# Optimization experiments

Hardware: AMD Instinct MI355X
Metric: run time of the kernel (lower is better)

## Reference

```python
import jax, jax.numpy as jnp
import numpy as np

N, E, NG = 50000, 800000, 500          # nodes, edges, graphs
HID, HEADS, DH, AIN = 128, 4, 32, 200  # hidden, heads, head dim, atom feat dim
L, NBASE = 5, 1                        # total Roost layers; base layers = roost_layers-3 = 1


def _bn(x, g, b):
    # BatchNorm1d in training mode: batch stats over axis 0 (biased var), affine
    m = x.mean(axis=0)
    v = x.var(axis=0)
    return g * (x - m) * jax.lax.rsqrt(v + 1e-5) + b


def _mlp(x, W, b, g, be):
    # MLPLayer = Linear -> BatchNorm1d -> SiLU
    return jax.nn.silu(_bn(x @ W + b, g, be))


def _roost(x, w, src, dst, Wf, bf, gf, bef, Wg, bg, gg, beg, gn, ben):
    n = x.shape[0]
    hihj = jnp.concatenate([x[src], x[dst]], axis=-1)            # [E, 2h]
    e = jnp.exp(_mlp(hihj, Wf, bf, gf, bef))                     # [E, 1]
    wexp = w[src] * e                                            # [E, 1] src weight * exp(e_ij)
    sum_w = jax.ops.segment_sum(wexp, dst, num_segments=n)       # [N, 1] dst-normalizer
    a = wexp / sum_w[dst]                                        # [E, 1] attention coeff
    z = jnp.einsum('ef,hfd->ehd', hihj, Wg) + bg                 # [E, H, dh] per-head linear
    z = jax.nn.silu(gg * (z - z.mean(axis=0)) * jax.lax.rsqrt(z.var(axis=0) + 1e-5) + beg)
    m = (a[:, :, None] * z).reshape(hihj.shape[0], HID)          # concat heads -> [E, h]
    h = jax.ops.segment_sum(m, dst, num_segments=n)              # scatter-sum to dst nodes
    return _bn(h, gn, ben) + x                                   # bn_nodes + residual


def setup_inputs() -> dict:
    ks = list(jax.random.split(jax.random.key(0), 16))
    f32 = jnp.float32
    return {
        "atom_features": jax.random.normal(ks[0], (N, AIN), f32),
        "node_weight": jax.random.uniform(ks[1], (N, 1), f32, minval=0.05, maxval=1.0),
        "eps": jax.random.normal(ks[2], (N, HID), f32),
        "src": jax.random.randint(ks[3], (E,), 0, N),
        "dst": jax.random.randint(ks[4], (E,), 0, N),
        "graph_ids": jnp.sort(jax.random.randint(ks[5], (N,), 0, NG)),
        "W_embed": jax.random.normal(ks[6], (AIN, HID), f32) / np.sqrt(AIN).astype(np.float32),
        "b_embed": jnp.zeros((HID,), f32),
        "g_embed": jnp.ones((HID,), f32),
        "be_embed": jnp.zeros((HID,), f32),
        "Wf": jax.random.normal(ks[7], (L, 2 * HID, 1), f32) / np.sqrt(2 * HID).astype(np.float32),
        "bf": jnp.zeros((L, 1), f32),
        "gf": jnp.ones((L, 1), f32),
        "bef": jnp.zeros((L, 1), f32),
        "Wg": jax.random.normal(ks[8], (L, HEADS, 2 * HID, DH), f32) / np.sqrt(2 * HID).astype(np.float32),
        "bg": jnp.zeros((L, HEADS, DH), f32),
        "gg": jnp.ones((L, HEADS, DH), f32),
        "beg": jnp.zeros((L, HEADS, DH), f32),
        "gn": jnp.ones((L, HID), f32),
        "ben": jnp.zeros((L, HID), f32),
        "W_mu": jax.random.normal(ks[9], (HID, HID), f32) / np.sqrt(HID).astype(np.float32),
        "b_mu": jnp.zeros((HID,), f32),
        "W_var": jax.random.normal(ks[10], (HID, HID), f32) * 0.01,
        "b_var": jnp.zeros((HID,), f32),
    }


def reference(atom_features, node_weight, eps, W_embed, b_embed, g_embed, be_embed,
              Wf, bf, gf, bef, Wg, bg, gg, beg, gn, ben,
              W_mu, b_mu, W_var, b_var, src, dst, graph_ids):
    x = _mlp(atom_features, W_embed, b_embed, g_embed, be_embed)  # atom_embedding
    for i in range(NBASE):                                        # base_modules
        x = _roost(x, node_weight, src, dst, Wf[i], bf[i], gf[i], bef[i],
                   Wg[i], bg[i], gg[i], beg[i], gn[i], ben[i])
    mu = x @ W_mu + b_mu
    logvar = x @ W_var + b_var
    x = eps * jnp.exp(0.5 * logvar) + mu                          # reparameterize
    for i in range(NBASE, L):                                     # module_layers
        x = _roost(x, node_weight, src, dst, Wf[i], bf[i], gf[i], bef[i],
                   Wg[i], bg[i], gg[i], beg[i], gn[i], ben[i])
    sums = jax.ops.segment_sum(x, graph_ids, num_segments=NG)     # AvgPooling
    cnt = jax.ops.segment_sum(jnp.ones((N,), x.dtype), graph_ids, num_segments=NG)
    xr = sums / jnp.maximum(cnt, 1.0)[:, None]
    kld = jnp.mean(-0.5 * jnp.sum(1.0 + logvar - mu * mu - jnp.exp(logvar), axis=1))
    return xr, kld
```

## Files before the change

kernel.cpp:

```cpp
#include <hip/hip_runtime.h>
#include <hip/hip_bf16.h>
#include <stdint.h>

#define HID 128
#define LAYERS 5

typedef __attribute__((ext_vector_type(8))) short short8;
typedef __attribute__((ext_vector_type(4))) float f32x4;

__device__ __forceinline__ float bf2f(unsigned int u16) {
  union { unsigned int i; float f; } c; c.i = u16 << 16; return c.f;
}
__device__ __forceinline__ unsigned short f2bf(float f) {
  union { float f; unsigned int i; } c; c.f = f;
  unsigned int r = c.i + 0x7fffu + ((c.i >> 16) & 1u);
  return (unsigned short)(r >> 16);
}
__device__ __forceinline__ float fexp(float x) {
  float r; asm("v_exp_f32 %0, %1" : "=v"(r) : "v"(x * 1.44269504f)); return r;
}
__device__ __forceinline__ float frcp(float x) {
  float r; asm("v_rcp_f32 %0, %1" : "=v"(r) : "v"(x)); return r;
}
__device__ __forceinline__ float siluf(float v) { return v * frcp(1.f + fexp(-v)); }

template<int KS, int NCT, bool BF16OUT>
__launch_bounds__(256)
__global__ void gemm_bf16_kernel(const unsigned short* __restrict__ A,
                                 const unsigned short* __restrict__ Bt,
                                 const float* __restrict__ bias,
                                 void* __restrict__ Cv, int M) {
  constexpr int K = KS * 32;
  constexpr int SLOTS = KS * 4;
  constexpr int SSTR = (SLOTS + 7) & ~7;
  __shared__ unsigned short wlds[NCT * 16 * SSTR * 8];
  for (int i = threadIdx.x; i < NCT * 16 * SLOTS; i += 256) {
    int col = i / SLOTS, slot = i % SLOTS;
    int phys = slot ^ (col & 7);
    *(uint4*)&wlds[(col * SSTR + phys) * 8] = *(const uint4*)(Bt + (size_t)col * K + slot * 8);
  }
  __syncthreads();
  int lane = threadIdx.x & 63, wid = threadIdx.x >> 6;
  int l15 = lane & 15, l4 = lane >> 4;
  int n0 = blockIdx.x * 64 + wid * 16;
  f32x4 acc[NCT];
  #pragma unroll
  for (int ct = 0; ct < NCT; ++ct) { f32x4 z = {0.f, 0.f, 0.f, 0.f}; acc[ct] = z; }
  int ar = n0 + l15; if (ar >= M) ar = M - 1;
  #pragma unroll
  for (int kk = 0; kk < KS; ++kk) {
    short8 af = *(const short8*)(A + (size_t)ar * K + kk * 32 + l4 * 8);
    #pragma unroll
    for (int ct = 0; ct < NCT; ++ct) {
      int col = ct * 16 + l15;
      int phys = (kk * 4 + l4) ^ (col & 7);
      short8 bfr = *(const short8*)&wlds[(col * SSTR + phys) * 8];
      acc[ct] = __builtin_amdgcn_mfma_f32_16x16x32_bf16(af, bfr, acc[ct], 0, 0, 0);
    }
  }
  #pragma unroll
  for (int ct = 0; ct < NCT; ++ct) {
    int col = ct * 16 + l15;
    #pragma unroll
    for (int j = 0; j < 4; ++j) {
      int n = n0 + l4 * 4 + j;
      if (n < M) {
        float v = acc[ct][j] + bias[col];
        if (BF16OUT) ((unsigned short*)Cv)[(size_t)n * (NCT * 16) + col] = f2bf(v);
        else         ((float*)Cv)[(size_t)n * (NCT * 16) + col] = v;
      }
    }
  }
}

__global__ void cast_atom_kernel(const float* __restrict__ atom, unsigned short* __restrict__ ab,
                                 int N, int AIN) {
  int n = blockIdx.x, k = threadIdx.x;
  if (n < N && k < 224)
    ab[(size_t)n * 224 + k] = f2bf(k < AIN ? atom[(size_t)n * AIN + k] : 0.f);
}
__global__ void prep_we_kernel(const float* __restrict__ W, unsigned short* __restrict__ Bt,
                               int AIN) {
  int i = blockIdx.x * 256 + threadIdx.x;
  if (i >= 128 * 224) return;
  int col = i / 224, k = i % 224;
  Bt[i] = f2bf(k < AIN ? W[(size_t)k * 128 + col] : 0.f);
}

__global__ void colstats_kernel(const float* __restrict__ in, int M, float* __restrict__ stats) {
  int f = threadIdx.x & 127;
  int rl = threadIdx.x >> 7;
  float s = 0, s2 = 0;
  for (int r = blockIdx.x * 2 + rl; r < M; r += gridDim.x * 2) {
    float v = in[(size_t)r * 128 + f];
    s += v; s2 += v * v;
  }
  __shared__ float l1[256], l2[256];
  l1[threadIdx.x] = s; l2[threadIdx.x] = s2;
  __syncthreads();
  if (rl == 0) {
    atomicAdd(&stats[f],       s  + l1[128 + f]);
    atomicAdd(&stats[128 + f], s2 + l2[128 + f]);
  }
}

template<bool SILU, bool RES>
__global__ void bn_act_kernel(const float* __restrict__ in, const float* __restrict__ stats,
                              const float* __restrict__ g, const float* __restrict__ be,
                              const float* __restrict__ resid, float invM,
                              float* __restrict__ xout, unsigned short* __restrict__ xbout,
                              size_t total) {
  int f = threadIdx.x & 127;
  float mean = stats[f] * invM;
  float var  = stats[128 + f] * invM - mean * mean;
  float sc = g[f] * rsqrtf(var + 1e-5f);
  float sh = be[f] - mean * sc;
  for (size_t i = (size_t)blockIdx.x * blockDim.x + threadIdx.x; i < total;
       i += (size_t)gridDim.x * blockDim.x) {
    float v = in[i] * sc + sh;
    if (SILU) v = siluf(v);
    if (RES)  v += resid[i];
    xout[i] = v;
    xbout[i] = f2bf(v);
  }
}

__global__ void hist_kernel(const int* __restrict__ ids, int* __restrict__ deg, int E) {
  for (int e = blockIdx.x * blockDim.x + threadIdx.x; e < E; e += gridDim.x * blockDim.x)
    atomicAdd(&deg[ids[e]], 1);
}

__global__ void scan_block_kernel(const int* __restrict__ in, int n,
                                  int* __restrict__ excl, int* __restrict__ totals) {
  __shared__ int tmp[256];
  int idx = blockIdx.x * 256 + threadIdx.x;
  int v = (idx < n) ? in[idx] : 0;
  tmp[threadIdx.x] = v;
  __syncthreads();
  for (int o = 1; o < 256; o <<= 1) {
    int t = (threadIdx.x >= o) ? tmp[threadIdx.x - o] : 0;
    __syncthreads();
    tmp[threadIdx.x] += t;
    __syncthreads();
  }
  if (idx < n) excl[idx] = tmp[threadIdx.x] - v;
  if (threadIdx.x == 255 && totals) totals[blockIdx.x] = tmp[255];
}

__global__ void scan_add_kernel(const int* __restrict__ excl, const int* __restrict__ tot_excl,
                                const int* __restrict__ indeg, int* __restrict__ cstart, int n) {
  int idx = blockIdx.x * 256 + threadIdx.x;
  if (idx < n) {
    int v = excl[idx] + tot_excl[blockIdx.x];
    cstart[idx] = v;
    if (idx == n - 1) cstart[n] = v + indeg[idx];
  }
}

__global__ void scatter_kernel(const int* __restrict__ src, const int* __restrict__ dst,
                               const int* __restrict__ cstart, int* __restrict__ fill,
                               int* __restrict__ csrc, int* __restrict__ cdst, int E) {
  for (int e = blockIdx.x * blockDim.x + threadIdx.x; e < E; e += gridDim.x * blockDim.x) {
    int d = dst[e];
    int pos = cstart[d] + atomicAdd(&fill[d], 1);
    csrc[pos] = src[e];
    cdst[pos] = d;
  }
}

__global__ void prep_wg_kernel(const float* __restrict__ WgL, const float* __restrict__ bgL,
                               unsigned short* __restrict__ Bt, float* __restrict__ bias) {
  int i = blockIdx.x * 256 + threadIdx.x;
  if (i < 256 * 128) {
    int col = i >> 7, k = i & 127;
    int c = col & 127, h = c >> 5, d = c & 31;
    int krow = (col < 128) ? k : 128 + k;
    Bt[i] = f2bf(WgL[((size_t)h * 256 + krow) * 32 + d]);
  }
  if (i < 256) bias[i] = (i < 128) ? 0.f : bgL[i - 128];
}

__global__ void prep_mv_kernel(const float* __restrict__ Wm, const float* __restrict__ Wv,
                               const float* __restrict__ bm, const float* __restrict__ bv,
                               unsigned short* __restrict__ Bt, float* __restrict__ bias) {
  int i = blockIdx.x * 256 + threadIdx.x;
  if (i < 256 * 128) {
    int col = i >> 7, k = i & 127;
    Bt[i] = f2bf(col < 128 ? Wm[(size_t)k * 128 + col] : Wv[(size_t)k * 128 + col - 128]);
  }
  if (i < 256) bias[i] = (i < 128) ? bm[i] : bv[i - 128];
}

__global__ void pq_kernel(const unsigned short* __restrict__ xb, const float* __restrict__ WfL,
                          const float* __restrict__ bfL, const int* __restrict__ indeg,
                          const int* __restrict__ outdeg, float* __restrict__ p,
                          float* __restrict__ q, float* __restrict__ gstats, int N) {
  __shared__ float wf[256];
  __shared__ float red1[4], red2[4];
  wf[threadIdx.x] = WfL[threadIdx.x];
  __syncthreads();
  int wid = threadIdx.x >> 6, lane = threadIdx.x & 63;
  int f0 = lane * 2;
  float bf0 = bfL[0];
  float t1 = 0, t2 = 0;
  for (int n = blockIdx.x * 4 + wid; n < N; n += gridDim.x * 4) {
    unsigned xv = *(const unsigned*)(xb + ((size_t)n << 7) + f0);
    float x0 = bf2f(xv & 0xffffu), x1 = bf2f(xv >> 16);
    float pp = x0 * wf[f0]       + x1 * wf[f0 + 1];
    float qq = x0 * wf[128 + f0] + x1 * wf[129 + f0];
    #pragma unroll
    for (int o = 32; o; o >>= 1) { pp += __shfl_down(pp, o); qq += __shfl_down(qq, o); }
    if (lane == 0) {
      qq += bf0;
      p[n] = pp; q[n] = qq;
      float od = (float)outdeg[n], id = (float)indeg[n];
      t1 += od * pp + id * qq;
      t2 += od * pp * pp + id * qq * qq;
    }
  }
  if (lane == 0) { red1[wid] = t1; red2[wid] = t2; }
  __syncthreads();
  if (threadIdx.x == 0) {
    atomicAdd(&gstats[0], red1[0] + red1[1] + red1[2] + red1[3]);
    atomicAdd(&gstats[1], red2[0] + red2[1] + red2[2] + red2[3]);
  }
}

__global__ void zstat_node_kernel(const unsigned short* __restrict__ UVb,
                                  const int* __restrict__ indeg, const int* __restrict__ outdeg,
                                  float* __restrict__ zstats, int N) {
  int lane = threadIdx.x & 63, g = threadIdx.x >> 6;
  int f0 = lane * 2, f1 = f0 + 1;
  float zs0 = 0, zq0 = 0, zs1 = 0, zq1 = 0;
  for (int n = blockIdx.x * 4 + g; n < N; n += gridDim.x * 4) {
    float od = (float)outdeg[n], id = (float)indeg[n];
    unsigned up = *(const unsigned*)(UVb + ((size_t)n << 8) + f0);
    unsigned vp = *(const unsigned*)(UVb + ((size_t)n << 8) + 128 + f0);
    float u0 = bf2f(up & 0xffffu), u1 = bf2f(up >> 16);
    float v0 = bf2f(vp & 0xffffu), v1 = bf2f(vp >> 16);
    zs0 += od * u0 + id * v0;  zq0 += od * u0 * u0 + id * v0 * v0;
    zs1 += od * u1 + id * v1;  zq1 += od * u1 * u1 + id * v1 * v1;
  }
  __shared__ float r1[4][128], r2[4][128];
  r1[g][f0] = zs0; r1[g][f1] = zs1;
  r2[g][f0] = zq0; r2[g][f1] = zq1;
  __syncthreads();
  if (threadIdx.x < 128) {
    int f = threadIdx.x;
    atomicAdd(&zstats[f],       r1[0][f] + r1[1][f] + r1[2][f] + r1[3][f]);
    atomicAdd(&zstats[128 + f], r2[0][f] + r2[1][f] + r2[2][f] + r2[3][f]);
  }
}

__global__ void xwalk_kernel(const unsigned short* __restrict__ UVb,
                             const int* __restrict__ csrc, const int* __restrict__ cdst,
                             const float* __restrict__ p, const float* __restrict__ q,
                             float* __restrict__ zc_parts, float* __restrict__ gc_parts, int E) {
  int lane = threadIdx.x & 63, wid = threadIdx.x >> 6;
  int gw = (blockIdx.x * 256 + threadIdx.x) >> 6;
  int nw = (gridDim.x * 256) >> 6;
  int f0 = lane * 2;
  float cr0 = 0, cr1 = 0, gc = 0;
  int nch = (E + 63) >> 6;
  for (int c = gw; c < nch; c += nw) {
    int e0 = c << 6, len = min(64, E - e0);
    int ee = e0 + (lane < len ? lane : len - 1);
    int idxs = csrc[ee], idxd = cdst[ee];
    if (lane < len) gc += p[idxs] * q[idxd];
    int dcur = __shfl(idxd, 0);
    float su0 = 0, su1 = 0;
    const unsigned short* base = UVb;
    #define LDU(i) (*(const unsigned*)(base + ((size_t)__shfl(idxs, (i) < len ? (i) : len - 1) << 8) + f0))
    unsigned a0 = LDU(0), a1 = LDU(1), a2 = LDU(2), a3 = LDU(3);
    for (int bs = 0; bs < len; bs += 4) {
      unsigned b0 = LDU(bs + 4), b1 = LDU(bs + 5), b2 = LDU(bs + 6), b3 = LDU(bs + 7);
      #define PROCX(i, up) if ((i) < len) {                                        \
        int d = __shfl(idxd, (i));                                                 \
        if (d != dcur) {                                                           \
          unsigned vp = *(const unsigned*)(base + ((size_t)dcur << 8) + 128 + f0); \
          cr0 += bf2f(vp & 0xffffu) * su0; cr1 += bf2f(vp >> 16) * su1;            \
          su0 = su1 = 0; dcur = d;                                                 \
        }                                                                          \
        su0 += bf2f((up) & 0xffffu); su1 += bf2f((up) >> 16); }
      PROCX(bs + 0, a0); PROCX(bs + 1, a1); PROCX(bs + 2, a2); PROCX(bs + 3, a3);
      a0 = b0; a1 = b1; a2 = b2; a3 = b3;
    }
    unsigned vp = *(const unsigned*)(base + ((size_t)dcur << 8) + 128 + f0);
    cr0 += bf2f(vp & 0xffffu) * su0; cr1 += bf2f(vp >> 16) * su1;
    #undef PROCX
    #undef LDU
  }
  __shared__ float r1[4][128], rg[4];
  #pragma unroll
  for (int o = 32; o; o >>= 1) gc += __shfl_down(gc, o);
  if (lane == 0) rg[wid] = gc;
  r1[wid][f0] = cr0; r1[wid][f0 + 1] = cr1;
  __syncthreads();
  if (threadIdx.x < 128) {
    int f = threadIdx.x;
    atomicAdd(&zc_parts[(blockIdx.x & 31) * 128 + f], r1[0][f] + r1[1][f] + r1[2][f] + r1[3][f]);
  }
  if (threadIdx.x == 0)
    atomicAdd(&gc_parts[blockIdx.x & 31], rg[0] + rg[1] + rg[2] + rg[3]);
}

__global__ void gate_wexp_kernel(const int* __restrict__ csrc, const int* __restrict__ cdst,
                                 const float* __restrict__ p, const float* __restrict__ q,
                                 const float* __restrict__ nodew, const float* __restrict__ gstats,
                                 const float* __restrict__ gc_parts,
                                 const float* __restrict__ gfL, const float* __restrict__ befL,
                                 float* __restrict__ wexp, float* __restrict__ sum_w,
                                 int E, float invE) {
  float gcr = 0;
  #pragma unroll
  for (int i = 0; i < 32; ++i) gcr += gc_parts[i];
  float gm  = gstats[0] * invE;
  float gv  = (gstats[1] + 2.f * gcr) * invE - gm * gm;
  float gsc = gfL[0] * rsqrtf(gv + 1e-5f);
  float gsh = befL[0] - gm * gsc;
  for (int e = blockIdx.x * blockDim.x + threadIdx.x; e < E; e += gridDim.x * blockDim.x) {
    int s = csrc[e], d = cdst[e];
    float v = (p[s] + q[d]) * gsc + gsh;
    v = v * frcp(1.f + fexp(-v));
    float we = nodew[s] * fexp(v);
    wexp[e] = we;
    atomicAdd(&sum_w[d], we);
  }
}

__global__ void walk2_kernel(const unsigned short* __restrict__ UVb,
                             const int* __restrict__ csrc, const int* __restrict__ cdst,
                             const float* __restrict__ wexp, const float* __restrict__ sum_w,
                             const float* __restrict__ zstats, const float* __restrict__ zc_parts,
                             const float* __restrict__ gg, const float* __restrict__ beg,
                             float* __restrict__ h, int E, float invE) {
  int lane = threadIdx.x & 63;
  int gw = (blockIdx.x * 256 + threadIdx.x) >> 6;
  int nw = (gridDim.x * 256) >> 6;
  int f0 = lane * 2, f1 = f0 + 1;
  float cr0 = 0, cr1 = 0;
  #pragma unroll
  for (int i2 = 0; i2 < 32; ++i2) { cr0 += zc_parts[i2 * 128 + f0]; cr1 += zc_parts[i2 * 128 + f1]; }
  float zm0 = zstats[f0] * invE;
  float zv0 = (zstats[128 + f0] + 2.f * cr0) * invE - zm0 * zm0;
  float sc0 = gg[f0] * rsqrtf(zv0 + 1e-5f), sh0 = beg[f0] - zm0 * sc0;
  float zm1 = zstats[f1] * invE;
  float zv1 = (zstats[128 + f1] + 2.f * cr1) * invE - zm1 * zm1;
  float sc1 = gg[f1] * rsqrtf(zv1 + 1e-5f), sh1 = beg[f1] - zm1 * sc1;

  int nch = (E + 63) >> 6;
  for (int c = gw; c < nch; c += nw) {
    int e0 = c << 6, len = min(64, E - e0);
    int ee = e0 + (lane < len ? lane : len - 1);
    int idxs = csrc[ee], idxd = cdst[ee];
    float wv = wexp[ee];
    int dcur = __shfl(idxd, 0);
    float inv = frcp(sum_w[dcur]);
    float c0, c1;
    { unsigned vp = *(const unsigned*)(UVb + ((size_t)dcur << 8) + 128 + f0);
      c0 = bf2f(vp & 0xffffu) * sc0 + sh0; c1 = bf2f(vp >> 16) * sc1 + sh1; }
    float h0 = 0, h1 = 0;
    #define LDU(i) (*(const unsigned*)(UVb + ((size_t)__shfl(idxs, (i) < len ? (i) : len - 1) << 8) + f0))
    unsigned a0 = LDU(0), a1 = LDU(1), a2 = LDU(2), a3 = LDU(3);
    for (int bs = 0; bs < len; bs += 4) {
      unsigned b0 = LDU(bs + 4), b1 = LDU(bs + 5), b2 = LDU(bs + 6), b3 = LDU(bs + 7);
      #define PROCW(i, up) if ((i) < len) {                                          \
        int d = __shfl(idxd, (i));                                                   \
        float a = __shfl(wv, (i));                                                   \
        if (d != dcur) {                                                             \
          atomicAdd(&h[((size_t)dcur << 7) + f0], h0 * inv);                         \
          atomicAdd(&h[((size_t)dcur << 7) + f1], h1 * inv);                         \
          h0 = h1 = 0; dcur = d; inv = frcp(sum_w[d]);                               \
          unsigned vp = *(const unsigned*)(UVb + ((size_t)d << 8) + 128 + f0);       \
          c0 = bf2f(vp & 0xffffu) * sc0 + sh0; c1 = bf2f(vp >> 16) * sc1 + sh1;      \
        }                                                                            \
        float v0 = bf2f((up) & 0xffffu) * sc0 + c0;                                  \
        float v1 = bf2f((up) >> 16)     * sc1 + c1;                                  \
        v0 = v0 * frcp(1.f + fexp(-v0));                                             \
        v1 = v1 * frcp(1.f + fexp(-v1));                                             \
        h0 += a * v0; h1 += a * v1; }
      PROCW(bs + 0, a0); PROCW(bs + 1, a1); PROCW(bs + 2, a2); PROCW(bs + 3, a3);
      a0 = b0; a1 = b1; a2 = b2; a3 = b3;
    }
    atomicAdd(&h[((size_t)dcur << 7) + f0], h0 * inv);
    atomicAdd(&h[((size_t)dcur << 7) + f1], h1 * inv);
    #undef PROCW
    #undef LDU
  }
}

__global__ void reparam_kernel(const unsigned short* __restrict__ muv,
                               const float* __restrict__ eps,
                               float* __restrict__ x, unsigned short* __restrict__ xb,
                               float* __restrict__ kacc, size_t total) {
  float part = 0;
  for (size_t i = (size_t)blockIdx.x * blockDim.x + threadIdx.x; i < total;
       i += (size_t)gridDim.x * blockDim.x) {
    size_t n = i >> 7; int f = (int)(i & 127);
    float m = bf2f(muv[(n << 8) + f]);
    float l = bf2f(muv[(n << 8) + 128 + f]);
    float el = fexp(l);
    float v = eps[i] * fexp(0.5f * l) + m;
    x[i] = v;
    xb[i] = f2bf(v);
    part += 1.f + l - m * m - el;
  }
  #pragma unroll
  for (int o = 32; o; o >>= 1) part += __shfl_down(part, o);
  __shared__ float la[4];
  int lane = threadIdx.x & 63, wid = threadIdx.x >> 6;
  if (lane == 0) la[wid] = part;
  __syncthreads();
  if (threadIdx.x == 0) atomicAdd(kacc, la[0] + la[1] + la[2] + la[3]);
}

__global__ void pool_kernel(const float* __restrict__ x, const int* __restrict__ gid,
                            float* __restrict__ pools, float* __restrict__ cnt, int N) {
  int lane = threadIdx.x & 63;
  int gw = (blockIdx.x * 256 + threadIdx.x) >> 6;
  int nw = (gridDim.x * 256) >> 6;
  int f0 = lane * 2, f1 = f0 + 1;
  const int CH = 64;
  int nch = (N + CH - 1) / CH;
  for (int c = gw; c < nch; c += nw) {
    int n0 = c * CH, n1 = min(N, n0 + CH);
    int gcur = gid[n0];
    float a0 = 0, a1 = 0, count = 0;
    for (int n = n0; n < n1; ++n) {
      int g = gid[n];
      if (g != gcur) {
        atomicAdd(&pools[((size_t)gcur << 7) + f0], a0);
        atomicAdd(&pools[((size_t)gcur << 7) + f1], a1);
        if (lane == 0) atomicAdd(&cnt[gcur], count);
        a0 = a1 = 0; count = 0; gcur = g;
      }
      float2 xv = *(const float2*)(x + ((size_t)n << 7) + f0);
      a0 += xv.x; a1 += xv.y; count += 1.f;
    }
    atomicAdd(&pools[((size_t)gcur << 7) + f0], a0);
    atomicAdd(&pools[((size_t)gcur << 7) + f1], a1);
    if (lane == 0) atomicAdd(&cnt[gcur], count);
  }
}

__global__ void finalize_kernel(const float* __restrict__ pools, const float* __restrict__ cnt,
                                const float* __restrict__ kacc, float* __restrict__ out,
                                int NG, float invN) {
  int i = blockIdx.x * blockDim.x + threadIdx.x;
  if (i < NG * 128) {
    float c = cnt[i >> 7];
    c = c > 1.f ? c : 1.f;
    out[i] = pools[i] / c;
  }
  if (i == 0) out[NG * 128] = -0.5f * kacc[0] * invN;
}

extern "C" void kernel_launch(void* const* d_in, const int* in_sizes, int n_in,
                              void* d_out, int out_size, void* d_ws, size_t ws_size,
                              hipStream_t stream) {
  const float* atom    = (const float*)d_in[0];
  const float* nodew   = (const float*)d_in[1];
  const float* epsp    = (const float*)d_in[2];
  const int*   src     = (const int*)d_in[3];
  const int*   dst     = (const int*)d_in[4];
  const int*   gid     = (const int*)d_in[5];
  const float* W_embed = (const float*)d_in[6];
  const float* b_embed = (const float*)d_in[7];
  const float* g_embed = (const float*)d_in[8];
  const float* be_embed= (const float*)d_in[9];
  const float* Wf      = (const float*)d_in[10];
  const float* bfp     = (const float*)d_in[11];
  const float* gfp     = (const float*)d_in[12];
  const float* befp    = (const float*)d_in[13];
  const float* Wg      = (const float*)d_in[14];
  const float* bg      = (const float*)d_in[15];
  const float* gg      = (const float*)d_in[16];
  const float* beg     = (const float*)d_in[17];
  const float* gn      = (const float*)d_in[18];
  const float* ben     = (const float*)d_in[19];
  const float* W_mu    = (const float*)d_in[20];
  const float* b_mu    = (const float*)d_in[21];
  const float* W_var   = (const float*)d_in[22];
  const float* b_var   = (const float*)d_in[23];

  const int N   = in_sizes[1];
  const int E   = in_sizes[3];
  const int AIN = in_sizes[0] / N;
  const int NG  = (out_size - 1) / HID;

  char* w = (char*)d_ws;
  size_t off = 0;
  auto alloc = [&](size_t bytes) { size_t r = off; off = (off + bytes + 255) & ~(size_t)255; return r; };
  size_t o_x    = alloc((size_t)N*HID*4);
  size_t o_xb   = alloc((size_t)N*HID*2);
  size_t o_uvb  = alloc((size_t)N*256*2);
  size_t o_h    = alloc((size_t)N*HID*4);
  size_t o_ab   = alloc((size_t)N*224*2);
  size_t o_p    = alloc((size_t)N*4);
  size_t o_q    = alloc((size_t)N*4);
  size_t o_sw   = alloc((size_t)N*4);
  size_t o_wexp = alloc((size_t)E*4);
  size_t o_csrc = alloc((size_t)E*4);
  size_t o_cdst = alloc((size_t)E*4);
  size_t o_cs   = alloc((size_t)(N+1)*4);
  size_t o_deg  = alloc((size_t)3*N*4);
  size_t o_excl = alloc((size_t)N*4);
  size_t o_tot  = alloc(512*4);
  size_t o_bt   = alloc((size_t)256*128*2);
  size_t o_bias = alloc(256*4);
  size_t o_st   = alloc((546 + 32*128)*4);
  size_t o_kp   = alloc((size_t)(64 + NG*HID + NG)*4);

  float* x              = (float*)(w + o_x);
  unsigned short* xb    = (unsigned short*)(w + o_xb);
  unsigned short* UVb   = (unsigned short*)(w + o_uvb);
  float* h              = (float*)(w + o_h);
  unsigned short* atomb = (unsigned short*)(w + o_ab);
  float* p              = (float*)(w + o_p);
  float* q              = (float*)(w + o_q);
  float* sum_w          = (float*)(w + o_sw);
  float* wexp           = (float*)(w + o_wexp);
  int*   csrc           = (int*)(w + o_csrc);
  int*   cdst           = (int*)(w + o_cdst);
  int*   cstart         = (int*)(w + o_cs);
  int*   indeg          = (int*)(w + o_deg);
  int*   fill           = indeg + N;
  int*   outdeg         = indeg + 2*N;
  int*   excl           = (int*)(w + o_excl);
  int*   totals         = (int*)(w + o_tot);
  int*   tot_excl       = totals + 256;
  unsigned short* Bt    = (unsigned short*)(w + o_bt);
  float* bias           = (float*)(w + o_bias);
  float* stats          = (float*)(w + o_st);
  float* gstats         = stats;
  float* gc_parts       = stats + 2;
  float* zstats         = stats + 34;
  float* nstats         = stats + 290;
  float* zc_parts       = stats + 546;
  float* kacc           = (float*)(w + o_kp);
  float* pools          = kacc + 64;
  float* cnt            = pools + (size_t)NG*HID;

  const dim3 B(256);
  const int mblk = (N + 63) / 64;
  const int nb1  = (N + 255) / 256;
  const float invN = 1.f / (float)N;
  const float invE = 1.f / (float)E;
  const size_t totalNH = (size_t)N * HID;
  const size_t st_bytes = (546 + 32*128) * 4;

  hipMemsetAsync(w + o_st, 0, st_bytes, stream);
  hipMemsetAsync(w + o_kp, 0, (64 + (size_t)NG*HID + NG)*4, stream);
  hipMemsetAsync(w + o_deg, 0, (size_t)3*N*4, stream);

  hist_kernel<<<dim3(1024), B, 0, stream>>>(dst, indeg, E);
  hist_kernel<<<dim3(1024), B, 0, stream>>>(src, outdeg, E);
  scan_block_kernel<<<dim3(nb1), B, 0, stream>>>(indeg, N, excl, totals);
  scan_block_kernel<<<dim3(1), B, 0, stream>>>(totals, nb1, tot_excl, nullptr);
  scan_add_kernel<<<dim3(nb1), B, 0, stream>>>(excl, tot_excl, indeg, cstart, N);
  scatter_kernel<<<dim3(1024), B, 0, stream>>>(src, dst, cstart, fill, csrc, cdst, E);

  cast_atom_kernel<<<dim3(N), B, 0, stream>>>(atom, atomb, N, AIN);
  prep_we_kernel<<<dim3(112), B, 0, stream>>>(W_embed, Bt, AIN);
  gemm_bf16_kernel<7, 8, false><<<dim3(mblk), B, 0, stream>>>(atomb, Bt, b_embed, h, N);
  colstats_kernel<<<dim3(512), B, 0, stream>>>(h, N, nstats);
  bn_act_kernel<true,false><<<dim3(2048), B, 0, stream>>>(h, nstats, g_embed, be_embed,
                                                          x, invN, x, xb, totalNH);

  for (int l = 0; l < LAYERS; ++l) {
    if (l == 1) {
      prep_mv_kernel<<<dim3(128), B, 0, stream>>>(W_mu, W_var, b_mu, b_var, Bt, bias);
      gemm_bf16_kernel<4, 16, true><<<dim3(mblk), B, 0, stream>>>(xb, Bt, bias, UVb, N);
      reparam_kernel<<<dim3(2048), B, 0, stream>>>(UVb, epsp, x, xb, kacc, totalNH);
    }
    prep_wg_kernel<<<dim3(128), B, 0, stream>>>(Wg + (size_t)l*4*256*32, bg + l*128, Bt, bias);
    hipMemsetAsync(w + o_st, 0, st_bytes, stream);
    hipMemsetAsync(w + o_h, 0, (size_t)N*HID*4, stream);
    hipMemsetAsync(w + o_sw, 0, (size_t)N*4, stream);
    gemm_bf16_kernel<4, 16, true><<<dim3(mblk), B, 0, stream>>>(xb, Bt, bias, UVb, N);
    pq_kernel<<<dim3(512), B, 0, stream>>>(xb, Wf + l*256, bfp + l, indeg, outdeg,
                                           p, q, gstats, N);
    xwalk_kernel<<<dim3(2048), B, 0, stream>>>(UVb, csrc, cdst, p, q, zc_parts, gc_parts, E);
    zstat_node_kernel<<<dim3(512), B, 0, stream>>>(UVb, indeg, outdeg, zstats, N);
    gate_wexp_kernel<<<dim3(1024), B, 0, stream>>>(csrc, cdst, p, q, nodew, gstats, gc_parts,
                                                   gfp + l, befp + l, wexp, sum_w, E, invE);
    walk2_kernel<<<dim3(2048), B, 0, stream>>>(UVb, csrc, cdst, wexp, sum_w, zstats, zc_parts,
                                               gg + l*128, beg + l*128, h, E, invE);
    colstats_kernel<<<dim3(512), B, 0, stream>>>(h, N, nstats);
    bn_act_kernel<false,true><<<dim3(2048), B, 0, stream>>>(h, nstats, gn + l*128, ben + l*128,
                                                            x, invN, x, xb, totalNH);
  }

  pool_kernel<<<dim3(256), B, 0, stream>>>(x, gid, pools, cnt, N);
  finalize_kernel<<<dim3((NG*HID + 255)/256), B, 0, stream>>>(pools, cnt, kacc,
                                                              (float*)d_out, NG, invN);
}
```

Baseline: 2.031 ms.

## Fuse gate/attention normalizer into edge walk and z-stats into GEMM epilogue

Removes the separate gate_wexp kernel by computing the edge gate weight inside walk2 and accumulating sum_w per destination there. Normalization by sum_w is deferred to the node-level colstats and bn_act kernels, so walk2 no longer needs sum_w ahead of time. The per-node z statistics move into the GEMM epilogue through shared-memory atomics, which drops the zstat_node kernel and a re-read of UVb. cdst is now filled from cstart instead of in the scatter, h and sum_w are cleared with one memset, and the wexp buffer is gone. In exchange, each edge recomputes the exp/silu gate inside the wider walk loop, and the GEMM gains extra LDS atomics.

```diff
diff --git a/kernel.cpp b/kernel.cpp
--- a/kernel.cpp
+++ b/kernel.cpp
@@ -24,12 +24,14 @@
 }
 __device__ __forceinline__ float siluf(float v) { return v * frcp(1.f + fexp(-v)); }
 
-template<int KS, int NCT, bool BF16OUT>
+template<int KS, int NCT, bool BF16OUT, bool ZSTAT>
 __launch_bounds__(256)
 __global__ void gemm_bf16_kernel(const unsigned short* __restrict__ A,
                                  const unsigned short* __restrict__ Bt,
                                  const float* __restrict__ bias,
-                                 void* __restrict__ Cv, int M) {
+                                 void* __restrict__ Cv, int M,
+                                 const int* __restrict__ indeg, const int* __restrict__ outdeg,
+                                 float* __restrict__ zstats) {
   constexpr int K = KS * 32;
   constexpr int SLOTS = KS * 4;
   constexpr int SSTR = (SLOTS + 7) & ~7;
@@ -71,6 +73,39 @@
       }
     }
   }
+  if constexpr (ZSTAT) {
+    __syncthreads();
+    float* zr = (float*)wlds;
+    for (int i = threadIdx.x; i < 512; i += 256) zr[i] = 0.f;
+    __syncthreads();
+    float odj[4], idj[4];
+    #pragma unroll
+    for (int j = 0; j < 4; ++j) {
+      int n = n0 + l4 * 4 + j;
+      odj[j] = (n < M) ? (float)outdeg[n] : 0.f;
+      idj[j] = (n < M) ? (float)indeg[n]  : 0.f;
+    }
+    #pragma unroll
+    for (int ct = 0; ct < NCT; ++ct) {
+      int col = ct * 16 + l15;
+      bool isv = col >= 128;
+      float s = 0, sq = 0;
+      #pragma unroll
+      for (int j = 0; j < 4; ++j) {
+        float v = acc[ct][j] + bias[col];
+        float w = isv ? idj[j] : odj[j];
+        s += w * v; sq += w * v * v;
+      }
+      atomicAdd(&zr[col], s);
+      atomicAdd(&zr[256 + col], sq);
+    }
+    __syncthreads();
+    if (threadIdx.x < 128) {
+      int f = threadIdx.x;
+      atomicAdd(&zstats[f],       zr[f]       + zr[128 + f]);
+      atomicAdd(&zstats[128 + f], zr[256 + f] + zr[384 + f]);
+    }
+  }
 }
 
 __global__ void cast_atom_kernel(const float* __restrict__ atom, unsigned short* __restrict__ ab,
@@ -87,12 +122,18 @@
   Bt[i] = f2bf(k < AIN ? W[(size_t)k * 128 + col] : 0.f);
 }
 
-__global__ void colstats_kernel(const float* __restrict__ in, int M, float* __restrict__ stats) {
+template<bool DIV>
+__global__ void colstats_kernel(const float* __restrict__ in, const float* __restrict__ sum_w,
+                                int M, float* __restrict__ stats) {
   int f = threadIdx.x & 127;
   int rl = threadIdx.x >> 7;
   float s = 0, s2 = 0;
   for (int r = blockIdx.x * 2 + rl; r < M; r += gridDim.x * 2) {
     float v = in[(size_t)r * 128 + f];
+    if (DIV) {
+      float sw = sum_w[r];
+      v *= (sw > 0.f) ? frcp(sw) : 0.f;
+    }
     s += v; s2 += v * v;
   }
   __shared__ float l1[256], l2[256];
@@ -104,8 +145,9 @@
   }
 }
 
-template<bool SILU, bool RES>
-__global__ void bn_act_kernel(const float* __restrict__ in, const float* __restrict__ stats,
+template<bool SILU, bool RES, bool DIV>
+__global__ void bn_act_kernel(const float* __restrict__ in, const float* __restrict__ sum_w,
+                              const float* __restrict__ stats,
                               const float* __restrict__ g, const float* __restrict__ be,
                               const float* __restrict__ resid, float invM,
                               float* __restrict__ xout, unsigned short* __restrict__ xbout,
@@ -117,7 +159,12 @@
   float sh = be[f] - mean * sc;
   for (size_t i = (size_t)blockIdx.x * blockDim.x + threadIdx.x; i < total;
        i += (size_t)gridDim.x * blockDim.x) {
-    float v = in[i] * sc + sh;
+    float hv = in[i];
+    if (DIV) {
+      float sw = sum_w[i >> 7];
+      hv *= (sw > 0.f) ? frcp(sw) : 0.f;
+    }
+    float v = hv * sc + sh;
     if (SILU) v = siluf(v);
     if (RES)  v += resid[i];
     xout[i] = v;
@@ -159,12 +206,18 @@
 
 __global__ void scatter_kernel(const int* __restrict__ src, const int* __restrict__ dst,
                                const int* __restrict__ cstart, int* __restrict__ fill,
-                               int* __restrict__ csrc, int* __restrict__ cdst, int E) {
+                               int* __restrict__ csrc, int E) {
   for (int e = blockIdx.x * blockDim.x + threadIdx.x; e < E; e += gridDim.x * blockDim.x) {
     int d = dst[e];
     int pos = cstart[d] + atomicAdd(&fill[d], 1);
     csrc[pos] = src[e];
-    cdst[pos] = d;
+  }
+}
+
+__global__ void fill_cdst_kernel(const int* __restrict__ cstart, int* __restrict__ cdst, int N) {
+  for (int n = blockIdx.x * blockDim.x + threadIdx.x; n < N; n += gridDim.x * blockDim.x) {
+    int s0 = cstart[n], s1 = cstart[n + 1];
+    for (int j = s0; j < s1; ++j) cdst[j] = n;
   }
 }
 
@@ -223,32 +276,6 @@
   if (threadIdx.x == 0) {
     atomicAdd(&gstats[0], red1[0] + red1[1] + red1[2] + red1[3]);
     atomicAdd(&gstats[1], red2[0] + red2[1] + red2[2] + red2[3]);
-  }
-}
-
-__global__ void zstat_node_kernel(const unsigned short* __restrict__ UVb,
-                                  const int* __restrict__ indeg, const int* __restrict__ outdeg,
-                                  float* __restrict__ zstats, int N) {
-  int lane = threadIdx.x & 63, g = threadIdx.x >> 6;
-  int f0 = lane * 2, f1 = f0 + 1;
-  float zs0 = 0, zq0 = 0, zs1 = 0, zq1 = 0;
-  for (int n = blockIdx.x * 4 + g; n < N; n += gridDim.x * 4) {
-    float od = (float)outdeg[n], id = (float)indeg[n];
-    unsigned up = *(const unsigned*)(UVb + ((size_t)n << 8) + f0);
-    unsigned vp = *(const unsigned*)(UVb + ((size_t)n << 8) + 128 + f0);
-    float u0 = bf2f(up & 0xffffu), u1 = bf2f(up >> 16);
-    float v0 = bf2f(vp & 0xffffu), v1 = bf2f(vp >> 16);
-    zs0 += od * u0 + id * v0;  zq0 += od * u0 * u0 + id * v0 * v0;
-    zs1 += od * u1 + id * v1;  zq1 += od * u1 * u1 + id * v1 * v1;
-  }
-  __shared__ float r1[4][128], r2[4][128];
-  r1[g][f0] = zs0; r1[g][f1] = zs1;
-  r2[g][f0] = zq0; r2[g][f1] = zq1;
-  __syncthreads();
-  if (threadIdx.x < 128) {
-    int f = threadIdx.x;
-    atomicAdd(&zstats[f],       r1[0][f] + r1[1][f] + r1[2][f] + r1[3][f]);
-    atomicAdd(&zstats[128 + f], r2[0][f] + r2[1][f] + r2[2][f] + r2[3][f]);
   }
 }
 
@@ -304,13 +331,20 @@
     atomicAdd(&gc_parts[blockIdx.x & 31], rg[0] + rg[1] + rg[2] + rg[3]);
 }
 
-__global__ void gate_wexp_kernel(const int* __restrict__ csrc, const int* __restrict__ cdst,
-                                 const float* __restrict__ p, const float* __restrict__ q,
-                                 const float* __restrict__ nodew, const float* __restrict__ gstats,
-                                 const float* __restrict__ gc_parts,
-                                 const float* __restrict__ gfL, const float* __restrict__ befL,
-                                 float* __restrict__ wexp, float* __restrict__ sum_w,
-                                 int E, float invE) {
+__global__ void walk2_kernel(const unsigned short* __restrict__ UVb,
+                             const int* __restrict__ csrc, const int* __restrict__ cdst,
+                             const float* __restrict__ p, const float* __restrict__ q,
+                             const float* __restrict__ nodew,
+                             const float* __restrict__ gstats, const float* __restrict__ gc_parts,
+                             const float* __restrict__ gfL, const float* __restrict__ befL,
+                             const float* __restrict__ zstats, const float* __restrict__ zc_parts,
+                             const float* __restrict__ gg, const float* __restrict__ beg,
+                             float* __restrict__ h, float* __restrict__ sum_w,
+                             int E, float invE) {
+  int lane = threadIdx.x & 63;
+  int gw = (blockIdx.x * 256 + threadIdx.x) >> 6;
+  int nw = (gridDim.x * 256) >> 6;
+  int f0 = lane * 2, f1 = f0 + 1;
   float gcr = 0;
   #pragma unroll
   for (int i = 0; i < 32; ++i) gcr += gc_parts[i];
@@ -318,26 +352,6 @@
   float gv  = (gstats[1] + 2.f * gcr) * invE - gm * gm;
   float gsc = gfL[0] * rsqrtf(gv + 1e-5f);
   float gsh = befL[0] - gm * gsc;
-  for (int e = blockIdx.x * blockDim.x + threadIdx.x; e < E; e += gridDim.x * blockDim.x) {
-    int s = csrc[e], d = cdst[e];
-    float v = (p[s] + q[d]) * gsc + gsh;
-    v = v * frcp(1.f + fexp(-v));
-    float we = nodew[s] * fexp(v);
-    wexp[e] = we;
-    atomicAdd(&sum_w[d], we);
-  }
-}
-
-__global__ void walk2_kernel(const unsigned short* __restrict__ UVb,
-                             const int* __restrict__ csrc, const int* __restrict__ cdst,
-                             const float* __restrict__ wexp, const float* __restrict__ sum_w,
-                             const float* __restrict__ zstats, const float* __restrict__ zc_parts,
-                             const float* __restrict__ gg, const float* __restrict__ beg,
-                             float* __restrict__ h, int E, float invE) {
-  int lane = threadIdx.x & 63;
-  int gw = (blockIdx.x * 256 + threadIdx.x) >> 6;
-  int nw = (gridDim.x * 256) >> 6;
-  int f0 = lane * 2, f1 = f0 + 1;
   float cr0 = 0, cr1 = 0;
   #pragma unroll
   for (int i2 = 0; i2 < 32; ++i2) { cr0 += zc_parts[i2 * 128 + f0]; cr1 += zc_parts[i2 * 128 + f1]; }
@@ -353,24 +367,26 @@
     int e0 = c << 6, len = min(64, E - e0);
     int ee = e0 + (lane < len ? lane : len - 1);
     int idxs = csrc[ee], idxd = cdst[ee];
-    float wv = wexp[ee];
+    float gt = (p[idxs] + q[idxd]) * gsc + gsh;
+    gt = gt * frcp(1.f + fexp(-gt));
+    float we = nodew[idxs] * fexp(gt);
     int dcur = __shfl(idxd, 0);
-    float inv = frcp(sum_w[dcur]);
     float c0, c1;
     { unsigned vp = *(const unsigned*)(UVb + ((size_t)dcur << 8) + 128 + f0);
       c0 = bf2f(vp & 0xffffu) * sc0 + sh0; c1 = bf2f(vp >> 16) * sc1 + sh1; }
-    float h0 = 0, h1 = 0;
+    float h0 = 0, h1 = 0, sw = 0;
     #define LDU(i) (*(const unsigned*)(UVb + ((size_t)__shfl(idxs, (i) < len ? (i) : len - 1) << 8) + f0))
     unsigned a0 = LDU(0), a1 = LDU(1), a2 = LDU(2), a3 = LDU(3);
     for (int bs = 0; bs < len; bs += 4) {
       unsigned b0 = LDU(bs + 4), b1 = LDU(bs + 5), b2 = LDU(bs + 6), b3 = LDU(bs + 7);
       #define PROCW(i, up) if ((i) < len) {                                          \
         int d = __shfl(idxd, (i));                                                   \
-        float a = __shfl(wv, (i));                                                   \
+        float a = __shfl(we, (i));                                                   \
         if (d != dcur) {                                                             \
-          atomicAdd(&h[((size_t)dcur << 7) + f0], h0 * inv);                         \
-          atomicAdd(&h[((size_t)dcur << 7) + f1], h1 * inv);                         \
-          h0 = h1 = 0; dcur = d; inv = frcp(sum_w[d]);                               \
+          atomicAdd(&h[((size_t)dcur << 7) + f0], h0);                               \
+          atomicAdd(&h[((size_t)dcur << 7) + f1], h1);                               \
+          if (lane == 0) atomicAdd(&sum_w[dcur], sw);                                \
+          h0 = h1 = 0; sw = 0; dcur = d;                                             \
           unsigned vp = *(const unsigned*)(UVb + ((size_t)d << 8) + 128 + f0);       \
           c0 = bf2f(vp & 0xffffu) * sc0 + sh0; c1 = bf2f(vp >> 16) * sc1 + sh1;      \
         }                                                                            \
@@ -378,12 +394,13 @@
         float v1 = bf2f((up) >> 16)     * sc1 + c1;                                  \
         v0 = v0 * frcp(1.f + fexp(-v0));                                             \
         v1 = v1 * frcp(1.f + fexp(-v1));                                             \
-        h0 += a * v0; h1 += a * v1; }
+        h0 += a * v0; h1 += a * v1; sw += a; }
       PROCW(bs + 0, a0); PROCW(bs + 1, a1); PROCW(bs + 2, a2); PROCW(bs + 3, a3);
       a0 = b0; a1 = b1; a2 = b2; a3 = b3;
     }
-    atomicAdd(&h[((size_t)dcur << 7) + f0], h0 * inv);
-    atomicAdd(&h[((size_t)dcur << 7) + f1], h1 * inv);
+    atomicAdd(&h[((size_t)dcur << 7) + f0], h0);
+    atomicAdd(&h[((size_t)dcur << 7) + f1], h1);
+    if (lane == 0) atomicAdd(&sum_w[dcur], sw);
     #undef PROCW
     #undef LDU
   }
@@ -494,12 +511,11 @@
   size_t o_x    = alloc((size_t)N*HID*4);
   size_t o_xb   = alloc((size_t)N*HID*2);
   size_t o_uvb  = alloc((size_t)N*256*2);
+  size_t o_sw   = alloc((size_t)N*4);
   size_t o_h    = alloc((size_t)N*HID*4);
   size_t o_ab   = alloc((size_t)N*224*2);
   size_t o_p    = alloc((size_t)N*4);
   size_t o_q    = alloc((size_t)N*4);
-  size_t o_sw   = alloc((size_t)N*4);
-  size_t o_wexp = alloc((size_t)E*4);
   size_t o_csrc = alloc((size_t)E*4);
   size_t o_cdst = alloc((size_t)E*4);
   size_t o_cs   = alloc((size_t)(N+1)*4);
@@ -514,12 +530,11 @@
   float* x              = (float*)(w + o_x);
   unsigned short* xb    = (unsigned short*)(w + o_xb);
   unsigned short* UVb   = (unsigned short*)(w + o_uvb);
+  float* sum_w          = (float*)(w + o_sw);
   float* h              = (float*)(w + o_h);
   unsigned short* atomb = (unsigned short*)(w + o_ab);
   float* p              = (float*)(w + o_p);
   float* q              = (float*)(w + o_q);
-  float* sum_w          = (float*)(w + o_sw);
-  float* wexp           = (float*)(w + o_wexp);
   int*   csrc           = (int*)(w + o_csrc);
   int*   cdst           = (int*)(w + o_cdst);
   int*   cstart         = (int*)(w + o_cs);
@@ -548,6 +563,7 @@
   const float invE = 1.f / (float)E;
   const size_t totalNH = (size_t)N * HID;
   const size_t st_bytes = (546 + 32*128) * 4;
+  const size_t swh_bytes = (o_h + (size_t)N*HID*4) - o_sw;
 
   hipMemsetAsync(w + o_st, 0, st_bytes, stream);
   hipMemsetAsync(w + o_kp, 0, (64 + (size_t)NG*HID + NG)*4, stream);
@@ -558,37 +574,39 @@
   scan_block_kernel<<<dim3(nb1), B, 0, stream>>>(indeg, N, excl, totals);
   scan_block_kernel<<<dim3(1), B, 0, stream>>>(totals, nb1, tot_excl, nullptr);
   scan_add_kernel<<<dim3(nb1), B, 0, stream>>>(excl, tot_excl, indeg, cstart, N);
-  scatter_kernel<<<dim3(1024), B, 0, stream>>>(src, dst, cstart, fill, csrc, cdst, E);
+  scatter_kernel<<<dim3(1024), B, 0, stream>>>(src, dst, cstart, fill, csrc, E);
+  fill_cdst_kernel<<<dim3(256), B, 0, stream>>>(cstart, cdst, N);
 
   cast_atom_kernel<<<dim3(N), B, 0, stream>>>(atom, atomb, N, AIN);
   prep_we_kernel<<<dim3(112), B, 0, stream>>>(W_embed, Bt, AIN);
-  gemm_bf16_kernel<7, 8, false><<<dim3(mblk), B, 0, stream>>>(atomb, Bt, b_embed, h, N);
-  colstats_kernel<<<dim3(512), B, 0, stream>>>(h, N, nstats);
-  bn_act_kernel<true,false><<<dim3(2048), B, 0, stream>>>(h, nstats, g_embed, be_embed,
-                                                          x, invN, x, xb, totalNH);
+  gemm_bf16_kernel<7, 8, false, false><<<dim3(mblk), B, 0, stream>>>(
+      atomb, Bt, b_embed, h, N, nullptr, nullptr, nullptr);
+  colstats_kernel<false><<<dim3(512), B, 0, stream>>>(h, nullptr, N, nstats);
+  bn_act_kernel<true,false,false><<<dim3(2048), B, 0, stream>>>(
+      h, nullptr, nstats, g_embed, be_embed, x, invN, x, xb, totalNH);
 
   for (int l = 0; l < LAYERS; ++l) {
     if (l == 1) {
       prep_mv_kernel<<<dim3(128), B, 0, stream>>>(W_mu, W_var, b_mu, b_var, Bt, bias);
-      gemm_bf16_kernel<4, 16, true><<<dim3(mblk), B, 0, stream>>>(xb, Bt, bias, UVb, N);
+      gemm_bf16_kernel<4, 16, true, false><<<dim3(mblk), B, 0, stream>>>(
+          xb, Bt, bias, UVb, N, nullptr, nullptr, nullptr);
       reparam_kernel<<<dim3(2048), B, 0, stream>>>(UVb, epsp, x, xb, kacc, totalNH);
     }
     prep_wg_kernel<<<dim3(128), B, 0, stream>>>(Wg + (size_t)l*4*256*32, bg + l*128, Bt, bias);
     hipMemsetAsync(w + o_st, 0, st_bytes, stream);
-    hipMemsetAsync(w + o_h, 0, (size_t)N*HID*4, stream);
-    hipMemsetAsync(w + o_sw, 0, (size_t)N*4, stream);
-    gemm_bf16_kernel<4, 16, true><<<dim3(mblk), B, 0, stream>>>(xb, Bt, bias, UVb, N);
+    hipMemsetAsync(w + o_sw, 0, swh_bytes, stream);
+    gemm_bf16_kernel<4, 16, true, true><<<dim3(mblk), B, 0, stream>>>(
+        xb, Bt, bias, UVb, N, indeg, outdeg, zstats);
     pq_kernel<<<dim3(512), B, 0, stream>>>(xb, Wf + l*256, bfp + l, indeg, outdeg,
                                            p, q, gstats, N);
     xwalk_kernel<<<dim3(2048), B, 0, stream>>>(UVb, csrc, cdst, p, q, zc_parts, gc_parts, E);
-    zstat_node_kernel<<<dim3(512), B, 0, stream>>>(UVb, indeg, outdeg, zstats, N);
-    gate_wexp_kernel<<<dim3(1024), B, 0, stream>>>(csrc, cdst, p, q, nodew, gstats, gc_parts,
-                                                   gfp + l, befp + l, wexp, sum_w, E, invE);
-    walk2_kernel<<<dim3(2048), B, 0, stream>>>(UVb, csrc, cdst, wexp, sum_w, zstats, zc_parts,
-                                               gg + l*128, beg + l*128, h, E, invE);
-    colstats_kernel<<<dim3(512), B, 0, stream>>>(h, N, nstats);
-    bn_act_kernel<false,true><<<dim3(2048), B, 0, stream>>>(h, nstats, gn + l*128, ben + l*128,
-                                                            x, invN, x, xb, totalNH);
+    walk2_kernel<<<dim3(2048), B, 0, stream>>>(UVb, csrc, cdst, p, q, nodew,
+                                               gstats, gc_parts, gfp + l, befp + l,
+                                               zstats, zc_parts, gg + l*128, beg + l*128,
+                                               h, sum_w, E, invE);
+    colstats_kernel<true><<<dim3(512), B, 0, stream>>>(h, sum_w, N, nstats);
+    bn_act_kernel<false,true,true><<<dim3(2048), B, 0, stream>>>(
+        h, sum_w, nstats, gn + l*128, ben + l*128, x, invN, x, xb, totalNH);
   }
 
   pool_kernel<<<dim3(256), B, 0, stream>>>(x, gid, pools, cnt, N);
```

Result: faster. 1.859 ms (-8.5%).
